# Kernel optimization log

Hardware: AMD Instinct MI355X
Metric: run time of the kernel (lower is better)

## Reference

```python
import jax, jax.numpy as jnp
import numpy as np

B, S = 4096, 4096
NEG_INF = -1e30


def _conv1d_same(x, w, pad):
    # x: [B, S], w: [K] -> cross-correlation with zero padding, like torch F.conv1d
    out = jax.lax.conv_general_dilated(
        x[:, None, :], w[None, None, :], (1,), [(pad, pad)],
        dimension_numbers=("NCH", "OIH", "NCH"))
    return out[:, 0, :]


def setup_inputs() -> dict:
    key = jax.random.key(0)
    kx, kl, k1, k2, k3 = jax.random.split(key, 5)
    x = jax.random.normal(kx, (B, S), dtype=jnp.float32)
    length = jax.random.randint(kl, (B,), 1, S + 1, dtype=jnp.int32)
    w1 = 0.01 * jax.random.normal(k1, (3,), dtype=jnp.float32)
    w2 = 0.01 * jax.random.normal(k2, (5,), dtype=jnp.float32)
    w3 = 0.01 * jax.random.normal(k3, (7,), dtype=jnp.float32)
    return {"x": x, "length": length, "w1": w1, "w2": w2, "w3": w3}


def reference(x, length, w1, w2, w3):
    # mask out padding beyond each sample's length; zeroing x beyond length makes
    # the 'same'-padded conv identical to per-sample conv on the truncated sequence
    pos = jnp.arange(S)
    mask = pos[None, :] < length[:, None]          # [B, S]
    xm = jnp.where(mask, x, 0.0)

    def branch(w, pad):
        logits = _conv1d_same(xm, w, pad)          # [B, S]
        logits = jnp.where(mask, logits, NEG_INF)  # softmax only over valid positions
        qw = jax.nn.softmax(logits, axis=-1)
        return jnp.sum(qw * xm, axis=-1)           # [B]

    s1 = branch(w1, 1)
    s2 = branch(w2, 2)
    s3 = branch(w3, 3)
    fused = (s1 + s2 + s3) / 3.0
    return fused[:, None]                          # [B, 1]
```

## Files before the change

kernel.cpp:

```cpp
#include <hip/hip_runtime.h>
#include <type_traits>

#define SEQ 4096
#define CHUNK 256

__global__ __launch_bounds__(64) void msr_kernel(
    const float* __restrict__ x, const int* __restrict__ length,
    const float* __restrict__ w1, const float* __restrict__ w2,
    const float* __restrict__ w3, float* __restrict__ out)
{
    const int row  = blockIdx.x;
    const int lane = threadIdx.x & 63;
    const int L    = length[row];

    const float a0=w1[0],a1=w1[1],a2=w1[2];
    const float b0=w2[0],b1=w2[1],b2=w2[2],b3=w2[3],b4=w2[4];
    const float c0=w3[0],c1=w3[1],c2=w3[2],c3=w3[3],c4=w3[4],c5=w3[5],c6=w3[6];

    const float4* __restrict__ xrow =
        reinterpret_cast<const float4*>(x + (size_t)row * SEQ);

    float d1=0.f,n1=0.f,d2=0.f,n2=0.f,d3=0.f,n3=0.f;
    float cax=0.f, cay=0.f, caz=0.f;

    auto load_chunk = [&](int it) -> float4 {
        float4 v = make_float4(0.f,0.f,0.f,0.f);
        const int start = it * CHUNK;
        if (start < L) {
            if (start + CHUNK <= L) {
                v = xrow[(it << 6) + lane];
            } else {
                const int e = start + (lane << 2);
                if (e < L) {
                    v = xrow[(it << 6) + lane];
                    if (e + 1 >= L) v.y = 0.f;
                    if (e + 2 >= L) v.z = 0.f;
                    if (e + 3 >= L) v.w = 0.f;
                }
            }
        }
        return v;
    };

    auto process = [&](const float4 v, const float4 vnext, int ebase, auto MASKED) {
        constexpr bool M = decltype(MASKED)::value;
        float Lm3 = __shfl_up(v.y, 1);
        float Lm2 = __shfl_up(v.z, 1);
        float Lm1 = __shfl_up(v.w, 1);
        if (lane == 0) { Lm3 = cax; Lm2 = cay; Lm1 = caz; }
        float Rp1 = __shfl_down(v.x, 1);
        float Rp2 = __shfl_down(v.y, 1);
        float Rp3 = __shfl_down(v.z, 1);
        const float nb0 = __shfl(vnext.x, 0);
        const float nb1 = __shfl(vnext.y, 0);
        const float nb2 = __shfl(vnext.z, 0);
        if (lane == 63) { Rp1 = nb0; Rp2 = nb1; Rp3 = nb2; }

        const float s[10] = {Lm3, Lm2, Lm1, v.x, v.y, v.z, v.w, Rp1, Rp2, Rp3};
        #pragma unroll
        for (int j = 0; j < 4; ++j) {
            const float xm3=s[j], xm2=s[j+1], xm1=s[j+2], x0=s[j+3],
                        xp1=s[j+4], xp2=s[j+5], xp3=s[j+6];
            const float l1 = fmaf(a0,xm1, fmaf(a1,x0, a2*xp1));
            const float l2 = fmaf(b0,xm2, fmaf(b1,xm1, fmaf(b2,x0,
                             fmaf(b3,xp1, b4*xp2))));
            const float l3 = fmaf(c0,xm3, fmaf(c1,xm2, fmaf(c2,xm1, fmaf(c3,x0,
                             fmaf(c4,xp1, fmaf(c5,xp2, c6*xp3))))));
            float E1 = __expf(l1), E2 = __expf(l2), E3 = __expf(l3);
            if (M) {
                const float msk = (ebase + (lane << 2) + j < L) ? 1.f : 0.f;
                E1 *= msk; E2 *= msk; E3 *= msk;
            }
            d1 += E1; n1 = fmaf(E1, x0, n1);
            d2 += E2; n2 = fmaf(E2, x0, n2);
            d3 += E3; n3 = fmaf(E3, x0, n3);
        }
        cax = __shfl(v.y, 63);
        cay = __shfl(v.z, 63);
        caz = __shfl(v.w, 63);
    };

    const int  nfull       = L >> 8;
    const bool has_partial = (L & (CHUNK - 1)) != 0;

    float4 vA = load_chunk(0);
    float4 vB = load_chunk(1);
    for (int it = 0; it < nfull; ++it) {
        float4 vC = load_chunk(it + 2);
        process(vA, vB, it * CHUNK, std::false_type{});
        vA = vB; vB = vC;
    }
    if (has_partial) {
        process(vA, vB, nfull * CHUNK, std::true_type{});
    }

    #pragma unroll
    for (int off = 32; off > 0; off >>= 1) {
        d1 += __shfl_xor(d1, off); n1 += __shfl_xor(n1, off);
        d2 += __shfl_xor(d2, off); n2 += __shfl_xor(n2, off);
        d3 += __shfl_xor(d3, off); n3 += __shfl_xor(n3, off);
    }
    if (lane == 0) {
        out[row] = (n1/d1 + n2/d2 + n3/d3) * (1.0f/3.0f);
    }
}

extern "C" void kernel_launch(void* const* d_in, const int* in_sizes, int n_in,
                              void* d_out, int out_size, void* d_ws, size_t ws_size,
                              hipStream_t stream) {
    const float* x      = (const float*)d_in[0];
    const int*   length = (const int*)d_in[1];
    const float* w1     = (const float*)d_in[2];
    const float* w2     = (const float*)d_in[3];
    const float* w3     = (const float*)d_in[4];
    float*       out    = (float*)d_out;
    const int    Bn     = in_sizes[1];
    msr_kernel<<<Bn, 64, 0, stream>>>(x, length, w1, w2, w3, out);
}
```

Measured before the change: 21.53 us.

## Split each row across four waves with overlapping halo loads and LDS reduction

Each row is now processed by a 256-thread block of four waves that interleave 256-element chunks, instead of one wave walking the whole row. Each lane loads its left and right neighbour float4s directly from memory instead of exchanging halos through cross-lane shuffles and carried registers. Per-wave partial sums are then combined through shared memory. This aims to raise memory-level parallelism and shorten the per-row serial chain, at the cost of three times the load instructions (mostly cache hits) and a block barrier.

```diff
diff --git a/kernel.cpp b/kernel.cpp
--- a/kernel.cpp
+++ b/kernel.cpp
@@ -1,97 +1,84 @@
 #include <hip/hip_runtime.h>
-#include <type_traits>
 
-#define SEQ 4096
+#define SEQ   4096
 #define CHUNK 256
+#define WPR   4
 
-__global__ __launch_bounds__(64) void msr_kernel(
+struct Ch { float4 vl, vm, vr; };
+
+__global__ __launch_bounds__(256) void msr_kernel(
     const float* __restrict__ x, const int* __restrict__ length,
     const float* __restrict__ w1, const float* __restrict__ w2,
     const float* __restrict__ w3, float* __restrict__ out)
 {
+    __shared__ float red[WPR][8];
+
     const int row  = blockIdx.x;
-    const int lane = threadIdx.x & 63;
+    const int tid  = threadIdx.x;
+    const int wave = tid >> 6;
+    const int lane = tid & 63;
     const int L    = length[row];
+    const int nch  = (L + CHUNK - 1) >> 8;
 
     const float a0=w1[0],a1=w1[1],a2=w1[2];
     const float b0=w2[0],b1=w2[1],b2=w2[2],b3=w2[3],b4=w2[4];
     const float c0=w3[0],c1=w3[1],c2=w3[2],c3=w3[3],c4=w3[4],c5=w3[5],c6=w3[6];
 
-    const float4* __restrict__ xrow =
-        reinterpret_cast<const float4*>(x + (size_t)row * SEQ);
+    const float* __restrict__ xr = x + (size_t)row * SEQ;
 
     float d1=0.f,n1=0.f,d2=0.f,n2=0.f,d3=0.f,n3=0.f;
-    float cax=0.f, cay=0.f, caz=0.f;
 
-    auto load_chunk = [&](int it) -> float4 {
-        float4 v = make_float4(0.f,0.f,0.f,0.f);
-        const int start = it * CHUNK;
-        if (start < L) {
-            if (start + CHUNK <= L) {
-                v = xrow[(it << 6) + lane];
-            } else {
-                const int e = start + (lane << 2);
-                if (e < L) {
-                    v = xrow[(it << 6) + lane];
-                    if (e + 1 >= L) v.y = 0.f;
-                    if (e + 2 >= L) v.z = 0.f;
-                    if (e + 3 >= L) v.w = 0.f;
-                }
-            }
+    auto load = [&](int it) -> Ch {
+        Ch c;
+        c.vl = make_float4(0.f,0.f,0.f,0.f);
+        c.vm = c.vl; c.vr = c.vl;
+        const int e = (it << 8) + (lane << 2);
+        if (e < L) {
+            c.vm = *reinterpret_cast<const float4*>(xr + e);
+            if (e >= 4)        c.vl = *reinterpret_cast<const float4*>(xr + e - 4);
+            if (e + 4 < SEQ)   c.vr = *reinterpret_cast<const float4*>(xr + e + 4);
         }
-        return v;
+        return c;
     };
 
-    auto process = [&](const float4 v, const float4 vnext, int ebase, auto MASKED) {
-        constexpr bool M = decltype(MASKED)::value;
-        float Lm3 = __shfl_up(v.y, 1);
-        float Lm2 = __shfl_up(v.z, 1);
-        float Lm1 = __shfl_up(v.w, 1);
-        if (lane == 0) { Lm3 = cax; Lm2 = cay; Lm1 = caz; }
-        float Rp1 = __shfl_down(v.x, 1);
-        float Rp2 = __shfl_down(v.y, 1);
-        float Rp3 = __shfl_down(v.z, 1);
-        const float nb0 = __shfl(vnext.x, 0);
-        const float nb1 = __shfl(vnext.y, 0);
-        const float nb2 = __shfl(vnext.z, 0);
-        if (lane == 63) { Rp1 = nb0; Rp2 = nb1; Rp3 = nb2; }
-
-        const float s[10] = {Lm3, Lm2, Lm1, v.x, v.y, v.z, v.w, Rp1, Rp2, Rp3};
+    auto proc = [&](const Ch c, int it) {
+        const int start = it << 8;
+        const int e     = start + (lane << 2);
+        float s[12] = {c.vl.x,c.vl.y,c.vl.z,c.vl.w,
+                       c.vm.x,c.vm.y,c.vm.z,c.vm.w,
+                       c.vr.x,c.vr.y,c.vr.z,c.vr.w};
+        const bool safe = (start + CHUNK + 4) <= L;
+        if (!safe) {
+            #pragma unroll
+            for (int k = 4; k < 12; ++k)
+                if (e - 4 + k >= L) s[k] = 0.f;
+        }
         #pragma unroll
         for (int j = 0; j < 4; ++j) {
-            const float xm3=s[j], xm2=s[j+1], xm1=s[j+2], x0=s[j+3],
-                        xp1=s[j+4], xp2=s[j+5], xp3=s[j+6];
+            const float xm3=s[j+1], xm2=s[j+2], xm1=s[j+3], x0=s[j+4],
+                        xp1=s[j+5], xp2=s[j+6], xp3=s[j+7];
             const float l1 = fmaf(a0,xm1, fmaf(a1,x0, a2*xp1));
             const float l2 = fmaf(b0,xm2, fmaf(b1,xm1, fmaf(b2,x0,
                              fmaf(b3,xp1, b4*xp2))));
             const float l3 = fmaf(c0,xm3, fmaf(c1,xm2, fmaf(c2,xm1, fmaf(c3,x0,
                              fmaf(c4,xp1, fmaf(c5,xp2, c6*xp3))))));
             float E1 = __expf(l1), E2 = __expf(l2), E3 = __expf(l3);
-            if (M) {
-                const float msk = (ebase + (lane << 2) + j < L) ? 1.f : 0.f;
-                E1 *= msk; E2 *= msk; E3 *= msk;
+            if (!safe) {
+                const float m = (e + j < L) ? 1.f : 0.f;
+                E1 *= m; E2 *= m; E3 *= m;
             }
             d1 += E1; n1 = fmaf(E1, x0, n1);
             d2 += E2; n2 = fmaf(E2, x0, n2);
             d3 += E3; n3 = fmaf(E3, x0, n3);
         }
-        cax = __shfl(v.y, 63);
-        cay = __shfl(v.z, 63);
-        caz = __shfl(v.w, 63);
     };
 
-    const int  nfull       = L >> 8;
-    const bool has_partial = (L & (CHUNK - 1)) != 0;
-
-    float4 vA = load_chunk(0);
-    float4 vB = load_chunk(1);
-    for (int it = 0; it < nfull; ++it) {
-        float4 vC = load_chunk(it + 2);
-        process(vA, vB, it * CHUNK, std::false_type{});
-        vA = vB; vB = vC;
-    }
-    if (has_partial) {
-        process(vA, vB, nfull * CHUNK, std::true_type{});
+    Ch A = load(wave);
+    Ch B = load(wave + WPR);
+    for (int it = wave; it < nch; it += WPR) {
+        Ch C = load(it + 2 * WPR);
+        proc(A, it);
+        A = B; B = C;
     }
 
     #pragma unroll
@@ -101,7 +88,18 @@
         d3 += __shfl_xor(d3, off); n3 += __shfl_xor(n3, off);
     }
     if (lane == 0) {
-        out[row] = (n1/d1 + n2/d2 + n3/d3) * (1.0f/3.0f);
+        red[wave][0]=d1; red[wave][1]=n1; red[wave][2]=d2;
+        red[wave][3]=n2; red[wave][4]=d3; red[wave][5]=n3;
+    }
+    __syncthreads();
+    if (tid == 0) {
+        float D1=0.f,N1=0.f,D2=0.f,N2=0.f,D3=0.f,N3=0.f;
+        #pragma unroll
+        for (int w = 0; w < WPR; ++w) {
+            D1+=red[w][0]; N1+=red[w][1]; D2+=red[w][2];
+            N2+=red[w][3]; D3+=red[w][4]; N3+=red[w][5];
+        }
+        out[row] = (N1/D1 + N2/D2 + N3/D3) * (1.0f/3.0f);
     }
 }
 
@@ -115,5 +113,5 @@
     const float* w3     = (const float*)d_in[4];
     float*       out    = (float*)d_out;
     const int    Bn     = in_sizes[1];
-    msr_kernel<<<Bn, 64, 0, stream>>>(x, length, w1, w2, w3, out);
+    msr_kernel<<<Bn, 256, 0, stream>>>(x, length, w1, w2, w3, out);
 }
```

Result: no change. 21.29 us, median of 2 (-1.2%).
